# Optimization experiments

Measured on AMD Instinct MI355X. Metric: run time of the kernel, lower is better.

## Reference

```python
import jax, jax.numpy as jnp
import numpy as np

N_SAMPLES = 1024   # self.n
B = 128            # batch of x
DIM = 64           # latent dim (self.dim)
DX = 64            # observation dim
K = 16             # annealing steps
N_LEAP = 3         # leapfrog inner steps
STEP = 0.05        # leapfrog step size
LOGVAR_P = 0.0     # momentum log-variance
LOG2PI = float(np.log(2.0 * np.pi))


def _betas():
    # beta_unnorm = sigmoid(4*(2*linspace(0,1,K+2)-1)); normalized to [0,1]
    b = jax.nn.sigmoid(4.0 * (2.0 * jnp.linspace(0.0, 1.0, K + 2) - 1.0))
    return (b - b[0]) / (b[-1] - b[0])


def _logprob_normal(z, logvar=0.0):
    return -0.5 * (LOG2PI + logvar + z * z * jnp.exp(-logvar))


def setup_inputs() -> dict:
    key = jax.random.key(0)
    k1, k2, k3, k4, k5 = jax.random.split(key, 5)
    x = jax.random.normal(k1, (B, DX), jnp.float32)
    W_enc = jax.random.normal(k2, (DX, DIM), jnp.float32) / jnp.sqrt(float(DX))
    W_dec = jax.random.normal(k3, (DIM, DX), jnp.float32) / jnp.sqrt(float(DIM))
    q_noise = jax.random.normal(k4, (N_SAMPLES, B, DIM), jnp.float32)
    p_noise = jax.random.normal(k5, (N_SAMPLES, B, DIM), jnp.float32)
    return {"x": x, "W_enc": W_enc, "W_dec": W_dec, "q_noise": q_noise, "p_noise": p_noise}


def reference(x, W_enc, W_dec, q_noise, p_noise):
    beta = _betas()
    mu = x @ W_enc  # (B, DIM) importance mean

    def loglik(q):  # Gaussian decoder logN(x | q @ W_dec, I), shape (n, B)
        r = jnp.einsum('nbd,de->nbe', q, W_dec)
        return _logprob_normal(x - r).sum(-1)

    def prior_lp(q):
        return _logprob_normal(q).sum(-1)

    def imp_lp(q):
        return _logprob_normal(q - mu).sum(-1)

    def w(q):  # functional: loglik + log prior - log importance
        return loglik(q) + prior_lp(q) - imp_lp(q)

    # initial samples from importance distr, initial momentum
    q0 = mu + q_noise                       # (n, B, DIM)
    p0 = jnp.exp(0.5 * LOGVAR_P) * p_noise  # (n, B, DIM)
    slw0 = (beta[1] - beta[0]) * w(q0)      # incremental weight at k=0

    noise_key = jax.random.key(42)

    def step(carry, inp):
        q, p, slw = carry
        bk, bkp1, kidx = inp
        # momentum refresh: v = 0 => full resample
        p = jnp.exp(0.5 * LOGVAR_P) * jax.random.normal(
            jax.random.fold_in(noise_key, kidx), q.shape, q.dtype)

        def tgt(qq):  # annealed target at beta_k (scalar for grad)
            return (bk * (loglik(qq) + prior_lp(qq)) + (1.0 - bk) * imp_lp(qq)).sum()

        g = jax.grad(tgt)
        for _ in range(N_LEAP):  # standard leapfrog
            p = p + 0.5 * STEP * g(q)
            q = q + STEP * p * jnp.exp(-LOGVAR_P)
            p = p + 0.5 * STEP * g(q)
        # NOTE: original torch accept/reject assignment is a no-op (chained
        # advanced indexing writes into a copy), so z_new is always kept.
        slw = slw + (bkp1 - bk) * w(q)
        return (q, p, slw), None

    ks = jnp.arange(1, K + 1)
    (qf, pf, slw), _ = jax.lax.scan(step, (q0, p0, slw0), (beta[1:K + 1], beta[2:K + 2], ks))
    return jax.scipy.special.logsumexp(slw, axis=0) - jnp.log(float(N_SAMPLES))
```

## Files before the change

### kernel.cpp

```cpp
#include <hip/hip_runtime.h>
#include <math.h>
#include <stdint.h>


#define WS_A     0
#define WS_MU    4096
#define WS_C     12288
#define WS_XSQ   20480
#define WS_AMU   20608
#define WS_F     28800
#define WS_WC    36992
#define WS_V     37120
#define WS_LAM   41216
#define WS_FZ    41280
#define WS_VF    49472
#define WS_SLW   53568
#define WS_TOTAL (WS_SLW + 131072)
#define WS_RNG   (WS_SLW + 131072)

#define LOG2PI 1.8378770664093453f

typedef _Float16 half8_t __attribute__((ext_vector_type(8)));
typedef float f4_t __attribute__((ext_vector_type(4)));
typedef unsigned int uint4_t __attribute__((ext_vector_type(4)));

struct KParams {
  float beta[18];
  float dbeta[17];
  uint32_t fk0[16];
  uint32_t fk1[16];
};

__host__ __device__ static inline void threefry2x32(uint32_t ks0, uint32_t ks1,
                                                    uint32_t x0, uint32_t x1,
                                                    uint32_t& o0, uint32_t& o1) {
  uint32_t ks2 = ks0 ^ ks1 ^ 0x1BD11BDAu;
  x0 += ks0; x1 += ks1;
#define TFR(r) { x0 += x1; x1 = (x1 << (r)) | (x1 >> (32 - (r))); x1 ^= x0; }
  TFR(13) TFR(15) TFR(26) TFR(6)
  x0 += ks1; x1 += ks2 + 1u;
  TFR(17) TFR(29) TFR(16) TFR(24)
  x0 += ks2; x1 += ks0 + 2u;
  TFR(13) TFR(15) TFR(26) TFR(6)
  x0 += ks0; x1 += ks1 + 3u;
  TFR(17) TFR(29) TFR(16) TFR(24)
  x0 += ks1; x1 += ks2 + 4u;
  TFR(13) TFR(15) TFR(26) TFR(6)
  x0 += ks2; x1 += ks0 + 5u;
#undef TFR
  o0 = x0; o1 = x1;
}

__device__ __forceinline__ float u_from_bits(uint32_t bits) {
  const float LO = __uint_as_float(0xBF7FFFFFu);
  float f = __uint_as_float((bits >> 9) | 0x3F800000u) - 1.0f;
  return fmaf(f, 2.0f, LO);
}

__device__ __forceinline__ float erfinv_f(float x) {
  float w = -__logf(fmaf(-x, x, 1.0f));
  float p;
  if (w < 5.0f) {
    w -= 2.5f;
    p = 2.81022636e-08f;
    p = fmaf(p, w, 3.43273939e-07f);
    p = fmaf(p, w, -3.5233877e-06f);
    p = fmaf(p, w, -4.39150654e-06f);
    p = fmaf(p, w, 0.00021858087f);
    p = fmaf(p, w, -0.00125372503f);
    p = fmaf(p, w, -0.00417768164f);
    p = fmaf(p, w, 0.246640727f);
    p = fmaf(p, w, 1.50140941f);
  } else {
    w = sqrtf(w) - 3.0f;
    p = -0.000200214257f;
    p = fmaf(p, w, 0.000100950558f);
    p = fmaf(p, w, 0.00134934322f);
    p = fmaf(p, w, -0.00367342844f);
    p = fmaf(p, w, 0.00573950773f);
    p = fmaf(p, w, -0.0076224613f);
    p = fmaf(p, w, 0.00943887047f);
    p = fmaf(p, w, 1.00167406f);
    p = fmaf(p, w, 2.83297682f);
  }
  return p * x;
}

__global__ void k_setup1(const float* __restrict__ x, const float* __restrict__ Wenc,
                         const float* __restrict__ Wdec, float* __restrict__ ws) {
  int t = blockIdx.x * 256 + threadIdx.x;
  if (t < 4096) {
    int i = t >> 6, j = t & 63;
    float s = 0;
    for (int e = 0; e < 64; ++e) s = fmaf(Wdec[i*64+e], Wdec[j*64+e], s);
    ws[WS_A + t] = s;
  } else if (t < 12288) {
    int u = t - 4096; int b = u >> 6, d = u & 63;
    float s = 0;
    for (int e = 0; e < 64; ++e) s = fmaf(x[b*64+e], Wenc[e*64+d], s);
    ws[WS_MU + u] = s;
  } else if (t < 20480) {
    int u = t - 12288; int b = u >> 6, d = u & 63;
    float s = 0;
    for (int e = 0; e < 64; ++e) s = fmaf(x[b*64+e], Wdec[d*64+e], s);
    ws[WS_C + u] = s;
  } else if (t < 20608) {
    int b = t - 20480;
    float s = 0;
    for (int e = 0; e < 64; ++e) s = fmaf(x[b*64+e], x[b*64+e], s);
    ws[WS_XSQ + b] = s;
  }
}

#define DRAW(PC, IDX)                                                        \
  { uint32_t o0, o1;                                                         \
    threefry2x32(k0, k1, 0u, base + (IDX), o0, o1);                          \
    PC = 1.41421356f * erfinv_f(u_from_bits(o0 ^ o1)); }

#define PACKD(DST, DD)                                                       \
  { _Float16 hh = (_Float16)(DD);                                            \
    _Float16 ll = (_Float16)((DD) - (float)hh);                              \
    DST = (uint32_t)__builtin_bit_cast(unsigned short, hh) |                 \
          ((uint32_t)__builtin_bit_cast(unsigned short, ll) << 16); }

#define EP 65
__global__ __launch_bounds__(1024) void k_fused(float* __restrict__ ws, KParams P,
                                                int nRng, int nS) {
  const int blk = blockIdx.x;
  const int tid = threadIdx.x;
  if (blk == 0) {
    __shared__ float Am[64 * EP];
    __shared__ float Vm[64 * EP];
    __shared__ float cs_c[32], cs_s[32];
    __shared__ int ppu[32], ppv[32];
    for (int i = tid; i < 4096; i += 1024) {
      int r = i >> 6, c = i & 63;
      Am[r*EP + c] = ws[WS_A + i];
      Vm[r*EP + c] = (r == c) ? 1.0f : 0.0f;
    }
    const int pA = tid & 31;
    int uA = (pA == 0) ? 0 : pA;
    int vA = (pA == 0) ? 63 : (63 - pA);
    const int pV0 = tid >> 6;
    int uV0 = (pV0 == 0) ? 0 : pV0;
    int vV0 = (pV0 == 0) ? 63 : (63 - pV0);
    const int pV1 = 16 + pV0;
    int uV1 = pV1;
    int vV1 = 63 - pV1;
    __syncthreads();
    for (int sweep = 0; sweep < 4; ++sweep) {
      for (int r = 0; r < 63; ++r) {
        if (tid < 32) {
          float app = Am[uA*(EP+1)], aqq = Am[vA*(EP+1)], apq = Am[uA*EP+vA];
          float c = 1.0f, s = 0.0f;
          if (fabsf(apq) > 1e-30f) {
            float tau = (aqq - app) / (2.0f * apq);
            float t = copysignf(1.0f / (fabsf(tau) + sqrtf(fmaf(tau, tau, 1.0f))), tau);
            c = 1.0f / sqrtf(fmaf(t, t, 1.0f));
            s = t * c;
          }
          ppu[tid] = uA; ppv[tid] = vA; cs_c[tid] = c; cs_s[tid] = s;
        }
        __syncthreads();
        {
          int i = tid >> 5;
          int ui = ppu[i], vi = ppv[i];
          const int uj = uA, vj = vA;
          float ci = cs_c[i], si = cs_s[i], cj = cs_c[pA], sj = cs_s[pA];
          float a = Am[ui*EP+uj], bb = Am[ui*EP+vj];
          float d = Am[vi*EP+uj], e  = Am[vi*EP+vj];
          float r0u = ci*a  - si*d;
          float r1u = fmaf(si, a,  ci*d);
          float r0v = ci*bb - si*e;
          float r1v = fmaf(si, bb, ci*e);
          Am[ui*EP+uj] = cj*r0u - sj*r0v;
          Am[ui*EP+vj] = fmaf(sj, r0u, cj*r0v);
          Am[vi*EP+uj] = cj*r1u - sj*r1v;
          Am[vi*EP+vj] = fmaf(sj, r1u, cj*r1v);
        }
        {
          const int k = tid & 63;
          {
            float c2 = cs_c[pV0], s2 = cs_s[pV0];
            float vu = Vm[k*EP+uV0], vv = Vm[k*EP+vV0];
            Vm[k*EP+uV0] = c2*vu - s2*vv;
            Vm[k*EP+vV0] = fmaf(s2, vu, c2*vv);
          }
          {
            float c2 = cs_c[pV1], s2 = cs_s[pV1];
            float vu = Vm[k*EP+uV1], vv = Vm[k*EP+vV1];
            Vm[k*EP+uV1] = c2*vu - s2*vv;
            Vm[k*EP+vV1] = fmaf(s2, vu, c2*vv);
          }
        }
        uA  = (uA  == 0) ? 0 : ((uA  == 63) ? 1 : uA  + 1);
        vA  = (vA  == 63) ? 1 : vA  + 1;
        uV0 = (uV0 == 0) ? 0 : ((uV0 == 63) ? 1 : uV0 + 1);
        vV0 = (vV0 == 63) ? 1 : vV0 + 1;
        uV1 = (uV1 == 63) ? 1 : uV1 + 1;
        vV1 = (vV1 == 63) ? 1 : vV1 + 1;
        __syncthreads();
      }
    }
    for (int i = tid; i < 4096; i += 1024) ws[WS_V + i] = Vm[(i >> 6)*EP + (i & 63)];
    if (tid < 64) ws[WS_LAM + tid] = Am[tid*(EP+1)];
  } else if (blk <= nRng) {
    const int L = (blk - 1) * 1024 + tid;
    const int bI = L >> 8, t256 = L & 255;
    const int wv = t256 >> 6, lane = t256 & 63;
    const int cw = lane & 15, g4 = lane >> 4;
    const int koff = g4 * 8;
    const int trajBase = bI * 64 + wv * 16;
    const uint32_t base = (uint32_t)(trajBase + cw) * 64u;
    uint32_t* wsu = (uint32_t*)ws;
    uint32_t* rngL = wsu + WS_RNG + (size_t)L * 16u * (unsigned)nS;
    for (int j = 1; j <= nS; ++j) {
      const uint32_t k0 = P.fk0[j-1], k1 = P.fk1[j-1];
      uint32_t ov[16];
#pragma unroll
      for (int i = 0; i < 8; ++i) { float dd; DRAW(dd, koff + i) PACKD(ov[i], dd) }
#pragma unroll
      for (int i = 0; i < 8; ++i) { float dd; DRAW(dd, 32 + koff + i) PACKD(ov[8+i], dd) }
      uint4_t* wr = (uint4_t*)(rngL + (size_t)(j-1)*16);
      wr[0] = (uint4_t){ov[0], ov[1], ov[2], ov[3]};
      wr[1] = (uint4_t){ov[4], ov[5], ov[6], ov[7]};
      wr[2] = (uint4_t){ov[8], ov[9], ov[10], ov[11]};
      wr[3] = (uint4_t){ov[12], ov[13], ov[14], ov[15]};
    }
  } else {
    int t = (blk - 1 - nRng) * 1024 + tid;
    if (t < 8192) {
      int b = t >> 6, d = t & 63;
      float s = 0;
      for (int m = 0; m < 64; ++m) s = fmaf(ws[WS_MU + b*64+m], ws[WS_A + m*64+d], s);
      ws[WS_AMU + t] = s;
      ws[WS_F + t] = ws[WS_C + t] - ws[WS_MU + t] - s;
    }
  }
}

__global__ void k_setupfv(float* __restrict__ ws) {
  int blk = blockIdx.x;
  if (blk < 32) {
    int t = blk * 256 + threadIdx.x;
    int b = t >> 6, d = t & 63;
    float s = 0;
    for (int m = 0; m < 64; ++m) s = fmaf(ws[WS_F + b*64+m], ws[WS_V + m*64+d], s);
    ws[WS_FZ + t] = s;
  } else if (blk < 36) {
    int idx = (blk - 32) * 256 + threadIdx.x;
    int lane = idx & 63, F = idx >> 6;
    int t = F >> 3, kt = (F >> 2) & 1, nt = F & 3;
    int n = nt*16 + (lane & 15);
    int k0 = kt*32 + ((lane >> 4) & 3)*8;
    uint32_t out[4];
    for (int jj = 0; jj < 4; ++jj) {
      float v0 = ws[WS_V + (k0 + 2*jj    )*64 + n];
      float v1 = ws[WS_V + (k0 + 2*jj + 1)*64 + n];
      _Float16 h0, h1;
      if (t == 0) { h0 = (_Float16)v0; h1 = (_Float16)v1; }
      else {
        _Float16 a0 = (_Float16)v0, a1 = (_Float16)v1;
        h0 = (_Float16)(v0 - (float)a0);
        h1 = (_Float16)(v1 - (float)a1);
      }
      unsigned short u0 = __builtin_bit_cast(unsigned short, h0);
      unsigned short u1 = __builtin_bit_cast(unsigned short, h1);
      out[jj] = (uint32_t)u0 | ((uint32_t)u1 << 16);
    }
    uint32_t* dst = (uint32_t*)ws + WS_VF + idx*4;
    dst[0] = out[0]; dst[1] = out[1]; dst[2] = out[2]; dst[3] = out[3];
  } else {
    int b = threadIdx.x;
    if (b < 128) {
      float muc = 0, musq = 0, muamu = 0;
      for (int d = 0; d < 64; ++d) {
        float m = ws[WS_MU + b*64+d];
        muc   = fmaf(m, ws[WS_C + b*64+d], muc);
        musq  = fmaf(m, m, musq);
        muamu = fmaf(m, ws[WS_AMU + b*64+d], muamu);
      }
      ws[WS_WC + b] = -32.0f * LOG2PI - 0.5f * ws[WS_XSQ + b]
                      + muc - 0.5f * musq - 0.5f * muamu;
    }
  }
}


#define SPLIT1(AH, AL, J, VV)                                                \
  { _Float16 hh = (_Float16)(VV); AH[J] = hh;                                \
    AL[J] = (_Float16)((VV) - (float)hh); }

#define DRAWSPLIT8(AH, AL, KB)                                               \
  { float dd;                                                                \
    DRAW(dd, (KB)+0) SPLIT1(AH, AL, 0, dd)                                   \
    DRAW(dd, (KB)+1) SPLIT1(AH, AL, 1, dd)                                   \
    DRAW(dd, (KB)+2) SPLIT1(AH, AL, 2, dd)                                   \
    DRAW(dd, (KB)+3) SPLIT1(AH, AL, 3, dd)                                   \
    DRAW(dd, (KB)+4) SPLIT1(AH, AL, 4, dd)                                   \
    DRAW(dd, (KB)+5) SPLIT1(AH, AL, 5, dd)                                   \
    DRAW(dd, (KB)+6) SPLIT1(AH, AL, 6, dd)                                   \
    DRAW(dd, (KB)+7) SPLIT1(AH, AL, 7, dd) }

#define FRAGB(T, KT, NT)                                                     \
  __builtin_bit_cast(half8_t, VF[(((T)*2+(KT))*4+(NT))*64 + lane])

#define ROT1(ZO, NT, AH0, AL0, AH1, AL1)                                     \
  { half8_t bh0 = FRAGB(0,0,NT), bh1 = FRAGB(0,1,NT);                        \
    half8_t bl0 = FRAGB(1,0,NT), bl1 = FRAGB(1,1,NT);                        \
    f4_t aa = {0.f, 0.f, 0.f, 0.f};                                          \
    aa = __builtin_amdgcn_mfma_f32_16x16x32_f16(AH0, bh0, aa, 0, 0, 0);      \
    aa = __builtin_amdgcn_mfma_f32_16x16x32_f16(AH1, bh1, aa, 0, 0, 0);      \
    aa = __builtin_amdgcn_mfma_f32_16x16x32_f16(AL0, bh0, aa, 0, 0, 0);      \
    aa = __builtin_amdgcn_mfma_f32_16x16x32_f16(AL1, bh1, aa, 0, 0, 0);      \
    aa = __builtin_amdgcn_mfma_f32_16x16x32_f16(AH0, bl0, aa, 0, 0, 0);      \
    aa = __builtin_amdgcn_mfma_f32_16x16x32_f16(AH1, bl1, aa, 0, 0, 0);      \
    ZO = aa; }

#define ROTATE4(O0, O1, O2, O3, AH0, AL0, AH1, AL1)                          \
  ROT1(O0, 0, AH0, AL0, AH1, AL1) ROT1(O1, 1, AH0, AL0, AH1, AL1)            \
  ROT1(O2, 2, AH0, AL0, AH1, AL1) ROT1(O3, 3, AH0, AL0, AH1, AL1)

#define LF4V(ZV, PV, NLM, FV, DBL)                                           \
  { f4_t gg = __builtin_elementwise_fma(bk4,                                 \
        __builtin_elementwise_fma(NLM, ZV, FV), -ZV);                        \
    PV = __builtin_elementwise_fma(c025v, gg, PV);                           \
    if (DBL) PV = __builtin_elementwise_fma(c025v, gg, PV);                  \
    ZV = __builtin_elementwise_fma(c005v, PV, ZV); }
#define SUBSTEPV(DBL)                                                        \
  LF4V(z0, pz0, nlm0, fzv0, DBL) LF4V(z1, pz1, nlm1, fzv1, DBL)              \
  LF4V(z2, pz2, nlm2, fzv2, DBL) LF4V(z3, pz3, nlm3, fzv3, DBL)

#define W_EVALN(WOUT)                                                        \
  { f4_t s1 = fzv0*z0 + fzv1*z1 + fzv2*z2 + fzv3*z3;                         \
    f4_t s2 = (lmS0*z0)*z0 + (lmS1*z1)*z1 + (lmS2*z2)*z2 + (lmS3*z3)*z3;     \
    f4_t vv = s1 - 0.5f*s2;                                                  \
    float r0 = vv.x, r1 = vv.y, r2 = vv.z, r3 = vv.w;                        \
    r0 += __shfl_xor(r0, 1); r1 += __shfl_xor(r1, 1);                        \
    r2 += __shfl_xor(r2, 1); r3 += __shfl_xor(r3, 1);                        \
    r0 += __shfl_xor(r0, 2); r1 += __shfl_xor(r1, 2);                        \
    r2 += __shfl_xor(r2, 2); r3 += __shfl_xor(r3, 2);                        \
    r0 += __shfl_xor(r0, 4); r1 += __shfl_xor(r1, 4);                        \
    r2 += __shfl_xor(r2, 4); r3 += __shfl_xor(r3, 4);                        \
    r0 += __shfl_xor(r0, 8); r1 += __shfl_xor(r1, 8);                        \
    r2 += __shfl_xor(r2, 8); r3 += __shfl_xor(r3, 8);                        \
    float wsel = (cw == 0) ? r0 : ((cw == 1) ? r1 : ((cw == 2) ? r2 : r3));  \
    WOUT = wsel + wcs; }

#define PLO 0x05040100u
#define PHI 0x07060302u

__global__ __launch_bounds__(256) void k_main(const float* __restrict__ qn,
                                              const float* __restrict__ ws,
                                              float* __restrict__ slw_out,
                                              KParams P, int nS) {
  __shared__ uint4_t VF[1024];
  const int tid = threadIdx.x;
  {
    const uint4_t* src = (const uint4_t*)((const uint32_t*)ws + WS_VF);
    for (int i = tid; i < 1024; i += 256) VF[i] = src[i];
  }
  __syncthreads();

  const int lane = tid & 63;
  const int wv = tid >> 6;
  const int cw = lane & 15;
  const int g4 = lane >> 4;
  const int koff = g4 * 8;
  const int trajBase = blockIdx.x * 64 + wv * 16;
  const uint32_t base = (uint32_t)(trajBase + cw) * 64u;
  const uint32_t* rngL = (const uint32_t*)ws + WS_RNG
                       + (size_t)(blockIdx.x * 256 + tid) * 16u * (unsigned)nS;

  const int b0 = (trajBase + g4*4 + 0) & 127;
  const int b1 = (trajBase + g4*4 + 1) & 127;
  const int b2 = (trajBase + g4*4 + 2) & 127;
  const int b3 = (trajBase + g4*4 + 3) & 127;
  f4_t fzv0, fzv1, fzv2, fzv3;
  fzv0.x = ws[WS_FZ + b0*64 + cw];      fzv0.y = ws[WS_FZ + b1*64 + cw];
  fzv0.z = ws[WS_FZ + b2*64 + cw];      fzv0.w = ws[WS_FZ + b3*64 + cw];
  fzv1.x = ws[WS_FZ + b0*64 + 16 + cw]; fzv1.y = ws[WS_FZ + b1*64 + 16 + cw];
  fzv1.z = ws[WS_FZ + b2*64 + 16 + cw]; fzv1.w = ws[WS_FZ + b3*64 + 16 + cw];
  fzv2.x = ws[WS_FZ + b0*64 + 32 + cw]; fzv2.y = ws[WS_FZ + b1*64 + 32 + cw];
  fzv2.z = ws[WS_FZ + b2*64 + 32 + cw]; fzv2.w = ws[WS_FZ + b3*64 + 32 + cw];
  fzv3.x = ws[WS_FZ + b0*64 + 48 + cw]; fzv3.y = ws[WS_FZ + b1*64 + 48 + cw];
  fzv3.z = ws[WS_FZ + b2*64 + 48 + cw]; fzv3.w = ws[WS_FZ + b3*64 + 48 + cw];
  const float lmS0 = ws[WS_LAM + cw];
  const float lmS1 = ws[WS_LAM + 16 + cw];
  const float lmS2 = ws[WS_LAM + 32 + cw];
  const float lmS3 = ws[WS_LAM + 48 + cw];
  const float wcs = ws[WS_WC + ((trajBase + g4*4 + (cw & 3)) & 127)];
  const f4_t nlm0 = {-lmS0, -lmS0, -lmS0, -lmS0};
  const f4_t nlm1 = {-lmS1, -lmS1, -lmS1, -lmS1};
  const f4_t nlm2 = {-lmS2, -lmS2, -lmS2, -lmS2};
  const f4_t nlm3 = {-lmS3, -lmS3, -lmS3, -lmS3};
  const f4_t c025v = {0.025f, 0.025f, 0.025f, 0.025f};
  const f4_t c005v = {0.05f, 0.05f, 0.05f, 0.05f};

  f4_t z0, z1, z2, z3, pz0, pz1, pz2, pz3;
  float slw = 0.0f;

  {
    const float* qp = qn + (size_t)base;
    f4_t qa = *(const f4_t*)(qp + koff);
    f4_t qb = *(const f4_t*)(qp + koff + 4);
    f4_t qc = *(const f4_t*)(qp + 32 + koff);
    f4_t qd = *(const f4_t*)(qp + 32 + koff + 4);
    half8_t ah0, al0, ah1, al1;
    SPLIT1(ah0, al0, 0, qa.x) SPLIT1(ah0, al0, 1, qa.y)
    SPLIT1(ah0, al0, 2, qa.z) SPLIT1(ah0, al0, 3, qa.w)
    SPLIT1(ah0, al0, 4, qb.x) SPLIT1(ah0, al0, 5, qb.y)
    SPLIT1(ah0, al0, 6, qb.z) SPLIT1(ah0, al0, 7, qb.w)
    SPLIT1(ah1, al1, 0, qc.x) SPLIT1(ah1, al1, 1, qc.y)
    SPLIT1(ah1, al1, 2, qc.z) SPLIT1(ah1, al1, 3, qc.w)
    SPLIT1(ah1, al1, 4, qd.x) SPLIT1(ah1, al1, 5, qd.y)
    SPLIT1(ah1, al1, 6, qd.z) SPLIT1(ah1, al1, 7, qd.w)
    ROTATE4(z0, z1, z2, z3, ah0, al0, ah1, al1)
  }
  {
    float w0;
    W_EVALN(w0);
    slw = fmaf(P.dbeta[0], w0, slw);
  }

  for (int j = 1; j <= 16; ++j) {
    const float bk = P.beta[j];
    const f4_t bk4 = {bk, bk, bk, bk};
    half8_t ah0, al0, ah1, al1;
    if (j <= nS) {
      const uint4_t* rr = (const uint4_t*)(rngL + (size_t)(j-1)*16);
      uint4_t q0 = rr[0], q1 = rr[1], q2 = rr[2], q3 = rr[3];
      uint4_t uh0 = { __builtin_amdgcn_perm(q0.y, q0.x, PLO),
                      __builtin_amdgcn_perm(q0.w, q0.z, PLO),
                      __builtin_amdgcn_perm(q1.y, q1.x, PLO),
                      __builtin_amdgcn_perm(q1.w, q1.z, PLO) };
      uint4_t ul0 = { __builtin_amdgcn_perm(q0.y, q0.x, PHI),
                      __builtin_amdgcn_perm(q0.w, q0.z, PHI),
                      __builtin_amdgcn_perm(q1.y, q1.x, PHI),
                      __builtin_amdgcn_perm(q1.w, q1.z, PHI) };
      uint4_t uh1 = { __builtin_amdgcn_perm(q2.y, q2.x, PLO),
                      __builtin_amdgcn_perm(q2.w, q2.z, PLO),
                      __builtin_amdgcn_perm(q3.y, q3.x, PLO),
                      __builtin_amdgcn_perm(q3.w, q3.z, PLO) };
      uint4_t ul1 = { __builtin_amdgcn_perm(q2.y, q2.x, PHI),
                      __builtin_amdgcn_perm(q2.w, q2.z, PHI),
                      __builtin_amdgcn_perm(q3.y, q3.x, PHI),
                      __builtin_amdgcn_perm(q3.w, q3.z, PHI) };
      ah0 = __builtin_bit_cast(half8_t, uh0);
      al0 = __builtin_bit_cast(half8_t, ul0);
      ah1 = __builtin_bit_cast(half8_t, uh1);
      al1 = __builtin_bit_cast(half8_t, ul1);
    } else {
      const uint32_t k0 = P.fk0[j-1], k1 = P.fk1[j-1];
      DRAWSPLIT8(ah0, al0, koff)
      DRAWSPLIT8(ah1, al1, 32 + koff)
    }
    ROTATE4(pz0, pz1, pz2, pz3, ah0, al0, ah1, al1)
    SUBSTEPV(false)
    SUBSTEPV(true)
    SUBSTEPV(true)
    float wj;
    W_EVALN(wj);
    slw = fmaf(P.dbeta[j], wj, slw);
  }
  if (cw < 4) slw_out[trajBase + g4*4 + cw] = slw;
}

__global__ void k_reduce(const float* __restrict__ slw, float* __restrict__ out) {
  __shared__ float red[256];
  int b = blockIdx.x, t = threadIdx.x;
  float v0 = slw[t*128 + b];
  float v1 = slw[(t+256)*128 + b];
  float v2 = slw[(t+512)*128 + b];
  float v3 = slw[(t+768)*128 + b];
  float m = fmaxf(fmaxf(v0, v1), fmaxf(v2, v3));
  red[t] = m; __syncthreads();
  for (int s = 128; s > 0; s >>= 1) {
    if (t < s) red[t] = fmaxf(red[t], red[t+s]);
    __syncthreads();
  }
  m = red[0]; __syncthreads();
  float sum = expf(v0 - m) + expf(v1 - m) + expf(v2 - m) + expf(v3 - m);
  red[t] = sum; __syncthreads();
  for (int s = 128; s > 0; s >>= 1) {
    if (t < s) red[t] += red[t+s];
    __syncthreads();
  }
  if (t == 0) out[b] = m + logf(red[0]) - 6.93147180559945309f;
}

extern "C" void kernel_launch(void* const* d_in, const int* in_sizes, int n_in,
                              void* d_out, int out_size, void* d_ws, size_t ws_size,
                              hipStream_t stream) {
  const float* x    = (const float*)d_in[0];
  const float* Wenc = (const float*)d_in[1];
  const float* Wdec = (const float*)d_in[2];
  const float* qn   = (const float*)d_in[3];
  float* ws  = (float*)d_ws;
  float* out = (float*)d_out;
  if (ws_size < (size_t)WS_TOTAL * sizeof(float)) return;

  size_t avail_u32 = ws_size / 4;
  int nS = 0;
  if (avail_u32 > (size_t)WS_RNG) {
    nS = (int)((avail_u32 - (size_t)WS_RNG) / 8388608ull);
    if (nS > 16) nS = 16;
  }
  const int nRng = (nS > 0) ? 512 : 0;

  KParams P;
  double bb[18];
  for (int i = 0; i < 18; ++i) {
    double tt = (double)i / 17.0;
    bb[i] = 1.0 / (1.0 + exp(-(8.0 * tt - 4.0)));
  }
  for (int i = 0; i < 18; ++i) P.beta[i] = (float)((bb[i] - bb[0]) / (bb[17] - bb[0]));
  for (int j = 0; j <= 16; ++j) P.dbeta[j] = P.beta[j+1] - P.beta[j];
  for (int k = 1; k <= 16; ++k) {
    uint32_t a, c;
    threefry2x32(0u, 42u, 0u, (uint32_t)k, a, c);
    P.fk0[k-1] = a; P.fk1[k-1] = c;
  }

  hipLaunchKernelGGL(k_setup1, dim3(81), dim3(256), 0, stream, x, Wenc, Wdec, ws);
  hipLaunchKernelGGL(k_fused, dim3(1 + nRng + 8), dim3(1024), 0, stream, ws, P, nRng, nS);
  hipLaunchKernelGGL(k_setupfv, dim3(37), dim3(256), 0, stream, ws);
  hipLaunchKernelGGL(k_main, dim3(2048), dim3(256), 0, stream, qn, ws, ws + WS_SLW, P, nS);
  hipLaunchKernelGGL(k_reduce, dim3(128), dim3(256), 0, stream, ws + WS_SLW, out);
}
```

Measured before the change: 621.9 us.

## Use step-major RNG layout, fill leftover workspace, cut Jacobi sweeps

After: 572.8 us. -7.9%, faster.

```diff
diff --git a/kernel.cpp b/kernel.cpp
--- a/kernel.cpp
+++ b/kernel.cpp
@@ -17,6 +17,7 @@
 #define WS_SLW   53568
 #define WS_TOTAL (WS_SLW + 131072)
 #define WS_RNG   (WS_SLW + 131072)
+#define STEP_U32 8388608ull
 
 #define LOG2PI 1.8378770664093453f
 
@@ -125,7 +126,7 @@
 
 #define EP 65
 __global__ __launch_bounds__(1024) void k_fused(float* __restrict__ ws, KParams P,
-                                                int nRng, int nS) {
+                                                int nRng, int nS, int Lcut) {
   const int blk = blockIdx.x;
   const int tid = threadIdx.x;
   if (blk == 0) {
@@ -148,7 +149,7 @@
     int uV1 = pV1;
     int vV1 = 63 - pV1;
     __syncthreads();
-    for (int sweep = 0; sweep < 4; ++sweep) {
+    for (int sweep = 0; sweep < 3; ++sweep) {
       for (int r = 0; r < 63; ++r) {
         if (tid < 32) {
           float app = Am[uA*(EP+1)], aqq = Am[vA*(EP+1)], apq = Am[uA*EP+vA];
@@ -213,15 +214,15 @@
     const int trajBase = bI * 64 + wv * 16;
     const uint32_t base = (uint32_t)(trajBase + cw) * 64u;
     uint32_t* wsu = (uint32_t*)ws;
-    uint32_t* rngL = wsu + WS_RNG + (size_t)L * 16u * (unsigned)nS;
-    for (int j = 1; j <= nS; ++j) {
+    const int nSteps = nS + ((nS < 16 && L < Lcut) ? 1 : 0);
+    for (int j = 1; j <= nSteps; ++j) {
       const uint32_t k0 = P.fk0[j-1], k1 = P.fk1[j-1];
       uint32_t ov[16];
 #pragma unroll
       for (int i = 0; i < 8; ++i) { float dd; DRAW(dd, koff + i) PACKD(ov[i], dd) }
 #pragma unroll
       for (int i = 0; i < 8; ++i) { float dd; DRAW(dd, 32 + koff + i) PACKD(ov[8+i], dd) }
-      uint4_t* wr = (uint4_t*)(rngL + (size_t)(j-1)*16);
+      uint4_t* wr = (uint4_t*)(wsu + WS_RNG + (size_t)(j-1)*STEP_U32 + (size_t)L*16u);
       wr[0] = (uint4_t){ov[0], ov[1], ov[2], ov[3]};
       wr[1] = (uint4_t){ov[4], ov[5], ov[6], ov[7]};
       wr[2] = (uint4_t){ov[8], ov[9], ov[10], ov[11]};
@@ -353,7 +354,7 @@
 __global__ __launch_bounds__(256) void k_main(const float* __restrict__ qn,
                                               const float* __restrict__ ws,
                                               float* __restrict__ slw_out,
-                                              KParams P, int nS) {
+                                              KParams P, int nS, int Lcut) {
   __shared__ uint4_t VF[1024];
   const int tid = threadIdx.x;
   {
@@ -369,8 +370,7 @@
   const int koff = g4 * 8;
   const int trajBase = blockIdx.x * 64 + wv * 16;
   const uint32_t base = (uint32_t)(trajBase + cw) * 64u;
-  const uint32_t* rngL = (const uint32_t*)ws + WS_RNG
-                       + (size_t)(blockIdx.x * 256 + tid) * 16u * (unsigned)nS;
+  const int Lme = blockIdx.x * 256 + tid;
 
   const int b0 = (trajBase + g4*4 + 0) & 127;
   const int b1 = (trajBase + g4*4 + 1) & 127;
@@ -427,8 +427,10 @@
     const float bk = P.beta[j];
     const f4_t bk4 = {bk, bk, bk, bk};
     half8_t ah0, al0, ah1, al1;
-    if (j <= nS) {
-      const uint4_t* rr = (const uint4_t*)(rngL + (size_t)(j-1)*16);
+    if (j <= nS || (j == nS + 1 && Lme < Lcut)) {
+      const uint32_t* rp = (const uint32_t*)ws + WS_RNG
+                         + (size_t)(j-1)*STEP_U32 + (size_t)Lme*16u;
+      const uint4_t* rr = (const uint4_t*)rp;
       uint4_t q0 = rr[0], q1 = rr[1], q2 = rr[2], q3 = rr[3];
       uint4_t uh0 = { __builtin_amdgcn_perm(q0.y, q0.x, PLO),
                       __builtin_amdgcn_perm(q0.w, q0.z, PLO),
@@ -501,12 +503,19 @@
   if (ws_size < (size_t)WS_TOTAL * sizeof(float)) return;
 
   size_t avail_u32 = ws_size / 4;
-  int nS = 0;
+  int nS = 0, Lcut = 0;
   if (avail_u32 > (size_t)WS_RNG) {
-    nS = (int)((avail_u32 - (size_t)WS_RNG) / 8388608ull);
+    size_t r = avail_u32 - (size_t)WS_RNG;
+    nS = (int)(r / STEP_U32);
     if (nS > 16) nS = 16;
-  }
-  const int nRng = (nS > 0) ? 512 : 0;
+    if (nS < 16) {
+      size_t rem = r - (size_t)nS * STEP_U32;
+      size_t lc = (rem / 16) & ~(size_t)63;
+      if (lc > 524288) lc = 524288;
+      Lcut = (int)lc;
+    }
+  }
+  const int nRng = (nS > 0 || Lcut > 0) ? 512 : 0;
 
   KParams P;
   double bb[18];
@@ -523,8 +532,8 @@
   }
 
   hipLaunchKernelGGL(k_setup1, dim3(81), dim3(256), 0, stream, x, Wenc, Wdec, ws);
-  hipLaunchKernelGGL(k_fused, dim3(1 + nRng + 8), dim3(1024), 0, stream, ws, P, nRng, nS);
+  hipLaunchKernelGGL(k_fused, dim3(1 + nRng + 8), dim3(1024), 0, stream, ws, P, nRng, nS, Lcut);
   hipLaunchKernelGGL(k_setupfv, dim3(37), dim3(256), 0, stream, ws);
-  hipLaunchKernelGGL(k_main, dim3(2048), dim3(256), 0, stream, qn, ws, ws + WS_SLW, P, nS);
+  hipLaunchKernelGGL(k_main, dim3(2048), dim3(256), 0, stream, qn, ws, ws + WS_SLW, P, nS, Lcut);
   hipLaunchKernelGGL(k_reduce, dim3(128), dim3(256), 0, stream, ws + WS_SLW, out);
 }
```
